# Performance work log

Measured on AMD Instinct MI355X. Metric: run time of the kernel, lower is better.

The kernel has to match this reference:

```python
import math
import jax, jax.numpy as jnp
import numpy as np

_EPS = 1e-6
N_DELTA, N_THETA, N_GAMMA = 4, 8, 16
N_OSC = N_DELTA + N_THETA + N_GAMMA  # 28
N_STEPS = 5
DT = 0.01
MATCH_THRESHOLD = 0.3
TWO_PI = 2.0 * math.pi

# Band natural frequencies (Hz): delta ~2, theta ~6, gamma ~40 (surrogate for DiscreteDeltaThetaGamma)
_OMEGA = TWO_PI * jnp.concatenate([
    jnp.full((N_DELTA,), 2.0, jnp.float32),
    jnp.full((N_THETA,), 6.0, jnp.float32),
    jnp.full((N_GAMMA,), 40.0, jnp.float32),
])


def setup_inputs() -> dict:
    key = jax.random.key(0)
    ks = jax.random.split(key, 12)
    N, D, H = 4096, 128, 64
    s1 = 1.0 / math.sqrt(D)
    s2 = 1.0 / math.sqrt(H)
    return {
        "detections_t": jax.random.normal(ks[0], (N, D), jnp.float32),
        "detections_t1": jax.random.normal(ks[1], (N, D), jnp.float32),
        # phase MLP
        "Wp1": jax.random.normal(ks[2], (D, H), jnp.float32) * s1,
        "bp1": jnp.zeros((H,), jnp.float32),
        "Wp2": jax.random.normal(ks[3], (H, N_OSC), jnp.float32) * s2,
        "bp2": jnp.zeros((N_OSC,), jnp.float32),
        # amplitude MLP
        "Wa1": jax.random.normal(ks[4], (D, H), jnp.float32) * s1,
        "ba1": jnp.zeros((H,), jnp.float32),
        "Wa2": jax.random.normal(ks[5], (H, N_OSC), jnp.float32) * s2,
        "ba2": jnp.zeros((N_OSC,), jnp.float32),
    }


def _encode(x, W1, b1, W2, b2, Wa1, ba1, Wa2, ba2):
    h = jax.nn.relu(x @ W1 + b1)
    phase = jnp.mod(h @ W2 + b2, TWO_PI)          # (N, n_osc)
    ha = jax.nn.relu(x @ Wa1 + ba1)
    amp = jax.nn.softplus(ha @ Wa2 + ba2)          # (N, n_osc)
    return phase, amp


def _evolve(phase, amp):
    # Kuramoto-style mean-field dynamics (surrogate for DiscreteDeltaThetaGamma.integrate)
    def step(carry, _):
        ph, am = carry
        c, s = jnp.cos(ph), jnp.sin(ph)
        mc = jnp.mean(c, axis=-1, keepdims=True)
        ms = jnp.mean(s, axis=-1, keepdims=True)
        # R*sin(psi - phi) = ms*cos(phi) - mc*sin(phi)
        coupling = ms * c - mc * s
        ph = jnp.mod(ph + DT * (_OMEGA + am * coupling), TWO_PI)
        return (ph, am), None
    (phase, amp), _ = jax.lax.scan(step, (phase, amp), None, length=N_STEPS)
    return phase, amp


def _phase_similarity(pa, pb):
    # sum_k cos(pa_k - pb_k) / (sqrt(K)+eps)^2, via real matmuls (no [Na,Nb,K] tensor)
    ca, sa = jnp.cos(pa), jnp.sin(pa)
    cb, sb = jnp.cos(pb), jnp.sin(pb)
    denom = (math.sqrt(N_OSC) + _EPS) ** 2
    return (ca @ cb.T + sa @ sb.T) / denom


def _greedy_match(sim, threshold):
    N_t, N_t1 = sim.shape
    max_sims = jnp.max(sim, axis=1)
    max_idxs = jnp.argmax(sim, axis=1)
    order = jnp.argsort(-max_sims)  # descending

    def step(used, idx):
        j = max_idxs[idx]
        ok = (~used[j]) & (max_sims[idx] > threshold)
        used = used.at[j].set(used[j] | ok)
        return used, jnp.where(ok, j, -1)

    used0 = jnp.zeros((N_t1,), bool)
    _, match_vals = jax.lax.scan(step, used0, order)
    matches = jnp.full((N_t,), -1, jnp.int32).at[order].set(match_vals.astype(jnp.int32))
    return matches


def reference(detections_t, detections_t1, Wp1, bp1, Wp2, bp2, Wa1, ba1, Wa2, ba2):
    phase_t, amp_t = _encode(detections_t, Wp1, bp1, Wp2, bp2, Wa1, ba1, Wa2, ba2)
    phase_t1, _ = _encode(detections_t1, Wp1, bp1, Wp2, bp2, Wa1, ba1, Wa2, ba2)
    phase_t_ev, _ = _evolve(phase_t, amp_t)
    sim = _phase_similarity(phase_t_ev, phase_t1)
    matches = _greedy_match(sim, MATCH_THRESHOLD)
    return matches, sim
```

## Files before the change

kernel.cpp:

```cpp
#include <hip/hip_runtime.h>
#include <math.h>

#define NDET 4096
#define DIM  128
#define HID  64
#define NOSC 28
#define KDIM 56

constexpr float TWO_PI_F = 6.28318530717958647692f;

__device__ __forceinline__ unsigned f2sort(float f){
    unsigned u = __float_as_uint(f);
    return (u & 0x80000000u) ? ~u : (u | 0x80000000u);
}
__device__ __forceinline__ float sort2f(unsigned u){
    return __uint_as_float((u & 0x80000000u) ? (u & 0x7fffffffu) : ~u);
}
__device__ __forceinline__ float lane_bcast(float v, int t){
    return __uint_as_float(__builtin_amdgcn_readlane(__float_as_uint(v), t));
}

__global__ __launch_bounds__(256) void encode_kernel(
    const float* __restrict__ det_t, const float* __restrict__ det_t1,
    const float* __restrict__ Wp1, const float* __restrict__ bp1,
    const float* __restrict__ Wp2, const float* __restrict__ bp2,
    const float* __restrict__ Wa1, const float* __restrict__ ba1,
    const float* __restrict__ Wa2, const float* __restrict__ ba2,
    float* __restrict__ At, float* __restrict__ Bt)
{
    const int tid  = threadIdx.x;
    const int lane = tid & 63;
    const int wv   = tid >> 6;
    const int b    = blockIdx.x;
    const bool isT = b < 512;
    const int lr = __builtin_amdgcn_readfirstlane(((b & 511) << 3) + wv * 2);
    const float* __restrict__ src = (isT ? det_t : det_t1) + (size_t)lr * DIM;

    float h0 = bp1[lane], h1 = h0;
    float g0 = 0.0f, g1 = 0.0f;
    if (isT){
        g0 = ba1[lane]; g1 = g0;
        #pragma unroll 8
        for (int d = 0; d < DIM; ++d){
            float x0 = src[d], x1 = src[DIM + d];
            float wp = Wp1[d * HID + lane];
            float wa = Wa1[d * HID + lane];
            h0 = fmaf(x0, wp, h0);  h1 = fmaf(x1, wp, h1);
            g0 = fmaf(x0, wa, g0);  g1 = fmaf(x1, wa, g1);
        }
        g0 = fmaxf(g0, 0.0f); g1 = fmaxf(g1, 0.0f);
    } else {
        #pragma unroll 8
        for (int d = 0; d < DIM; ++d){
            float x0 = src[d], x1 = src[DIM + d];
            float wp = Wp1[d * HID + lane];
            h0 = fmaf(x0, wp, h0);  h1 = fmaf(x1, wp, h1);
        }
    }
    h0 = fmaxf(h0, 0.0f); h1 = fmaxf(h1, 0.0f);

    const int k  = lane & 31;
    const bool kv = k < NOSC;
    const int kc = kv ? k : 0;

    float pa = bp2[kc], pb = pa;
    #pragma unroll 16
    for (int t = 0; t < HID; ++t){
        float w2 = Wp2[t * NOSC + kc];
        pa = fmaf(lane_bcast(h0, t), w2, pa);
        pb = fmaf(lane_bcast(h1, t), w2, pb);
    }
    float aa = 0.0f, ab = 0.0f;
    if (isT){
        aa = ba2[kc]; ab = aa;
        #pragma unroll 16
        for (int t = 0; t < HID; ++t){
            float w2 = Wa2[t * NOSC + kc];
            aa = fmaf(lane_bcast(g0, t), w2, aa);
            ab = fmaf(lane_bcast(g1, t), w2, ab);
        }
    }

    const bool hiHalf = lane >= 32;
    float p2 = hiHalf ? pb : pa;
    float ph = fmodf(p2, TWO_PI_F);
    if (ph < 0.0f) ph += TWO_PI_F;

    if (isT){
        float a2 = hiHalf ? ab : aa;
        float am = fmaxf(a2, 0.0f) + log1pf(expf(-fabsf(a2)));
        const float omega = TWO_PI_F * ((k < 4) ? 2.0f : (k < 12) ? 6.0f : 40.0f);
        for (int s5 = 0; s5 < 5; ++s5){
            float sn, cs;
            sincosf(ph, &sn, &cs);
            float c = kv ? cs : 0.0f;
            float s = kv ? sn : 0.0f;
            float sc = c, ss = s;
            sc += __shfl_xor(sc, 16); ss += __shfl_xor(ss, 16);
            sc += __shfl_xor(sc,  8); ss += __shfl_xor(ss,  8);
            sc += __shfl_xor(sc,  4); ss += __shfl_xor(ss,  4);
            sc += __shfl_xor(sc,  2); ss += __shfl_xor(ss,  2);
            sc += __shfl_xor(sc,  1); ss += __shfl_xor(ss,  1);
            float mc = sc * (1.0f / NOSC);
            float ms = ss * (1.0f / NOSC);
            float coupling = ms * c - mc * s;
            ph += 0.01f * (omega + am * coupling);
            ph = fmodf(ph, TWO_PI_F);
            if (ph < 0.0f) ph += TWO_PI_F;
        }
    }

    if (kv){
        const int row = lr + (hiHalf ? 1 : 0);
        float sn, cs;
        sincosf(ph, &sn, &cs);
        float* __restrict__ dst = isT ? At : Bt;
        dst[k * NDET + row]          = cs;
        dst[(NOSC + k) * NDET + row] = sn;
    }
}

__global__ __launch_bounds__(256, 4) void sim_kernel(
    const float* __restrict__ At, const float* __restrict__ Bt,
    float* __restrict__ sim_out, unsigned long long* __restrict__ rowmax)
{
    __shared__ float As[28][128];
    __shared__ float Bs[28][128];

    const int tid  = threadIdx.x;
    const int lane = tid & 63;
    const int wid  = tid >> 6;
    const int i0 = blockIdx.y * 128;
    const int j0 = blockIdx.x * 128;
    const int row0 = (wid & 1) * 64 + (lane & 7) * 8;
    const int col0 = (wid >> 1) * 64 + ((lane >> 3) & 7) * 8;

    float acc[8][8] = {};

    for (int chunk = 0; chunk < 2; ++chunk){
        const int kb = chunk * 28;
        if (chunk) __syncthreads();
        for (int v = tid; v < 28 * 32; v += 256){
            int kk = v >> 5, c4 = (v & 31) << 2;
            *(float4*)&As[kk][c4] = *(const float4*)&At[(size_t)(kb + kk) * NDET + i0 + c4];
            *(float4*)&Bs[kk][c4] = *(const float4*)&Bt[(size_t)(kb + kk) * NDET + j0 + c4];
        }
        __syncthreads();

        #pragma unroll 4
        for (int kk = 0; kk < 28; ++kk){
            float4 a0 = *(float4*)&As[kk][row0];
            float4 a1 = *(float4*)&As[kk][row0 + 4];
            float4 b0 = *(float4*)&Bs[kk][col0];
            float4 b1 = *(float4*)&Bs[kk][col0 + 4];
            float a[8]  = {a0.x, a0.y, a0.z, a0.w, a1.x, a1.y, a1.z, a1.w};
            float bb[8] = {b0.x, b0.y, b0.z, b0.w, b1.x, b1.y, b1.z, b1.w};
            #pragma unroll
            for (int r = 0; r < 8; ++r)
                #pragma unroll
                for (int c = 0; c < 8; ++c)
                    acc[r][c] = fmaf(a[r], bb[c], acc[r][c]);
        }
    }

    const float inv_denom =
        (float)(1.0 / ((5.2915026221291814 + 1e-6) * (5.2915026221291814 + 1e-6)));

    #pragma unroll
    for (int r = 0; r < 8; ++r){
        const int i = i0 + row0 + r;
        float vals[8];
        #pragma unroll
        for (int c = 0; c < 8; ++c) vals[c] = acc[r][c] * inv_denom;

        *(float4*)&sim_out[(size_t)i * NDET + j0 + col0]     =
            make_float4(vals[0], vals[1], vals[2], vals[3]);
        *(float4*)&sim_out[(size_t)i * NDET + j0 + col0 + 4] =
            make_float4(vals[4], vals[5], vals[6], vals[7]);

        float bv = vals[0]; int bj = j0 + col0;
        #pragma unroll
        for (int c = 1; c < 8; ++c)
            if (vals[c] > bv){ bv = vals[c]; bj = j0 + col0 + c; }
        unsigned long long key =
            ((unsigned long long)f2sort(bv) << 32) | (unsigned)(NDET - 1 - bj);
        #pragma unroll
        for (int m = 8; m <= 32; m <<= 1){
            unsigned long long o = __shfl_xor(key, m);
            if (o > key) key = o;
        }
        if (((lane >> 3) & 7) == 0) atomicMax(&rowmax[i], key);
    }
}

__global__ __launch_bounds__(256) void claim_kernel(
    const unsigned long long* __restrict__ rowmax,
    unsigned long long* __restrict__ colwin)
{
    int i = blockIdx.x * 256 + threadIdx.x;
    if (i >= NDET) return;
    unsigned long long key = rowmax[i];
    unsigned hi = (unsigned)(key >> 32);
    float v = sort2f(hi);
    if (v > 0.3f){
        int j = NDET - 1 - (int)(key & 0xffffffffu);
        unsigned long long ck = ((unsigned long long)hi << 32) | (unsigned)(NDET - 1 - i);
        atomicMax(&colwin[j], ck);
    }
}

__global__ __launch_bounds__(256) void finalize_kernel(
    const unsigned long long* __restrict__ rowmax,
    const unsigned long long* __restrict__ colwin,
    float* __restrict__ matches)
{
    int i = blockIdx.x * 256 + threadIdx.x;
    if (i >= NDET) return;
    unsigned long long key = rowmax[i];
    unsigned hi = (unsigned)(key >> 32);
    float v = sort2f(hi);
    int j = NDET - 1 - (int)(key & 0xffffffffu);
    unsigned long long ck = ((unsigned long long)hi << 32) | (unsigned)(NDET - 1 - i);
    bool ok = (v > 0.3f) && (colwin[j] == ck);
    matches[i] = ok ? (float)j : -1.0f;
}

extern "C" void kernel_launch(void* const* d_in, const int* in_sizes, int n_in,
                              void* d_out, int out_size, void* d_ws, size_t ws_size,
                              hipStream_t stream)
{
    const float* det_t  = (const float*)d_in[0];
    const float* det_t1 = (const float*)d_in[1];
    const float* Wp1 = (const float*)d_in[2];
    const float* bp1 = (const float*)d_in[3];
    const float* Wp2 = (const float*)d_in[4];
    const float* bp2 = (const float*)d_in[5];
    const float* Wa1 = (const float*)d_in[6];
    const float* ba1 = (const float*)d_in[7];
    const float* Wa2 = (const float*)d_in[8];
    const float* ba2 = (const float*)d_in[9];

    float* out     = (float*)d_out;
    float* matches = out;
    float* sim     = out + NDET;

    char* ws = (char*)d_ws;
    unsigned long long* rowmax = (unsigned long long*)ws;
    unsigned long long* colwin = (unsigned long long*)(ws + 32768);
    float* At = (float*)(ws + 65536);
    float* Bt = At + KDIM * NDET;

    hipMemsetAsync(d_ws, 0, 65536, stream);

    encode_kernel<<<1024, 256, 0, stream>>>(
        det_t, det_t1, Wp1, bp1, Wp2, bp2, Wa1, ba1, Wa2, ba2, At, Bt);

    sim_kernel<<<dim3(NDET / 128, NDET / 128), 256, 0, stream>>>(At, Bt, sim, rowmax);

    claim_kernel<<<NDET / 256, 256, 0, stream>>>(rowmax, colwin);
    finalize_kernel<<<NDET / 256, 256, 0, stream>>>(rowmax, colwin, matches);
}
```

Measured before the change: 157.8 us.

## Use split-fp16 MFMA for similarity GEMM and merge match kernels

The fp32 FMA similarity GEMM is replaced by MFMA 16x16x32 f16 instructions. Each operand is split into hi and lo fp16 parts and three products are summed to keep near-fp32 accuracy. The encode kernel now writes row-major fp16 hi/lo arrays padded to K=64, and sim_kernel loads fragments straight from global memory without LDS. The claim and finalize kernels are merged into one single-block kernel that keeps column winners in LDS, which removes a launch and part of the memset. The risk is that the split-fp16 precision error could flip the argmax on near-ties.

```diff
diff --git a/kernel.cpp b/kernel.cpp
--- a/kernel.cpp
+++ b/kernel.cpp
@@ -5,9 +5,12 @@
 #define DIM  128
 #define HID  64
 #define NOSC 28
-#define KDIM 56
+#define KPAD 64
 
 constexpr float TWO_PI_F = 6.28318530717958647692f;
+
+typedef _Float16 f16x8 __attribute__((ext_vector_type(8)));
+typedef float    f32x4 __attribute__((ext_vector_type(4)));
 
 __device__ __forceinline__ unsigned f2sort(float f){
     unsigned u = __float_as_uint(f);
@@ -26,7 +29,8 @@
     const float* __restrict__ Wp2, const float* __restrict__ bp2,
     const float* __restrict__ Wa1, const float* __restrict__ ba1,
     const float* __restrict__ Wa2, const float* __restrict__ ba2,
-    float* __restrict__ At, float* __restrict__ Bt)
+    _Float16* __restrict__ Ahi, _Float16* __restrict__ Alo,
+    _Float16* __restrict__ Bhi, _Float16* __restrict__ Blo)
 {
     const int tid  = threadIdx.x;
     const int lane = tid & 63;
@@ -110,119 +114,146 @@
         }
     }
 
+    const int row = lr + (hiHalf ? 1 : 0);
+    _Float16* __restrict__ dhi = isT ? Ahi : Bhi;
+    _Float16* __restrict__ dlo = isT ? Alo : Blo;
+    const size_t rb = (size_t)row * KPAD;
     if (kv){
-        const int row = lr + (hiHalf ? 1 : 0);
         float sn, cs;
         sincosf(ph, &sn, &cs);
-        float* __restrict__ dst = isT ? At : Bt;
-        dst[k * NDET + row]          = cs;
-        dst[(NOSC + k) * NDET + row] = sn;
-    }
-}
-
-__global__ __launch_bounds__(256, 4) void sim_kernel(
-    const float* __restrict__ At, const float* __restrict__ Bt,
+        _Float16 ch = (_Float16)cs;
+        _Float16 sh = (_Float16)sn;
+        _Float16 cl = (_Float16)(cs - (float)ch);
+        _Float16 sl = (_Float16)(sn - (float)sh);
+        dhi[rb + k]        = ch;
+        dhi[rb + NOSC + k] = sh;
+        dlo[rb + k]        = cl;
+        dlo[rb + NOSC + k] = sl;
+    } else {
+        const int kk = k - NOSC;
+        dhi[rb + 56 + kk] = (_Float16)0.0f;
+        dhi[rb + 60 + kk] = (_Float16)0.0f;
+        dlo[rb + 56 + kk] = (_Float16)0.0f;
+        dlo[rb + 60 + kk] = (_Float16)0.0f;
+    }
+}
+
+__global__ __launch_bounds__(256) void sim_kernel(
+    const _Float16* __restrict__ Ahi, const _Float16* __restrict__ Alo,
+    const _Float16* __restrict__ Bhi, const _Float16* __restrict__ Blo,
     float* __restrict__ sim_out, unsigned long long* __restrict__ rowmax)
 {
-    __shared__ float As[28][128];
-    __shared__ float Bs[28][128];
-
     const int tid  = threadIdx.x;
     const int lane = tid & 63;
     const int wid  = tid >> 6;
-    const int i0 = blockIdx.y * 128;
-    const int j0 = blockIdx.x * 128;
-    const int row0 = (wid & 1) * 64 + (lane & 7) * 8;
-    const int col0 = (wid >> 1) * 64 + ((lane >> 3) & 7) * 8;
-
-    float acc[8][8] = {};
-
-    for (int chunk = 0; chunk < 2; ++chunk){
-        const int kb = chunk * 28;
-        if (chunk) __syncthreads();
-        for (int v = tid; v < 28 * 32; v += 256){
-            int kk = v >> 5, c4 = (v & 31) << 2;
-            *(float4*)&As[kk][c4] = *(const float4*)&At[(size_t)(kb + kk) * NDET + i0 + c4];
-            *(float4*)&Bs[kk][c4] = *(const float4*)&Bt[(size_t)(kb + kk) * NDET + j0 + c4];
-        }
-        __syncthreads();
-
-        #pragma unroll 4
-        for (int kk = 0; kk < 28; ++kk){
-            float4 a0 = *(float4*)&As[kk][row0];
-            float4 a1 = *(float4*)&As[kk][row0 + 4];
-            float4 b0 = *(float4*)&Bs[kk][col0];
-            float4 b1 = *(float4*)&Bs[kk][col0 + 4];
-            float a[8]  = {a0.x, a0.y, a0.z, a0.w, a1.x, a1.y, a1.z, a1.w};
-            float bb[8] = {b0.x, b0.y, b0.z, b0.w, b1.x, b1.y, b1.z, b1.w};
-            #pragma unroll
-            for (int r = 0; r < 8; ++r)
-                #pragma unroll
-                for (int c = 0; c < 8; ++c)
-                    acc[r][c] = fmaf(a[r], bb[c], acc[r][c]);
-        }
-    }
+    const int i0 = blockIdx.y * 128 + (wid & 1) * 64;
+    const int j0 = blockIdx.x * 128 + (wid >> 1) * 64;
+    const int r16 = lane & 15;
+    const int g   = lane >> 4;
+
+    f16x8 ahi[4][2], alo[4][2];
+    #pragma unroll
+    for (int ib = 0; ib < 4; ++ib)
+        #pragma unroll
+        for (int kc = 0; kc < 2; ++kc){
+            const size_t off = (size_t)(i0 + ib*16 + r16) * KPAD + kc*32 + g*8;
+            ahi[ib][kc] = *(const f16x8*)&Ahi[off];
+            alo[ib][kc] = *(const f16x8*)&Alo[off];
+        }
 
     const float inv_denom =
         (float)(1.0 / ((5.2915026221291814 + 1e-6) * (5.2915026221291814 + 1e-6)));
 
-    #pragma unroll
-    for (int r = 0; r < 8; ++r){
-        const int i = i0 + row0 + r;
-        float vals[8];
-        #pragma unroll
-        for (int c = 0; c < 8; ++c) vals[c] = acc[r][c] * inv_denom;
-
-        *(float4*)&sim_out[(size_t)i * NDET + j0 + col0]     =
-            make_float4(vals[0], vals[1], vals[2], vals[3]);
-        *(float4*)&sim_out[(size_t)i * NDET + j0 + col0 + 4] =
-            make_float4(vals[4], vals[5], vals[6], vals[7]);
-
-        float bv = vals[0]; int bj = j0 + col0;
-        #pragma unroll
-        for (int c = 1; c < 8; ++c)
-            if (vals[c] > bv){ bv = vals[c]; bj = j0 + col0 + c; }
+    float bv[4] = {-3.4e38f, -3.4e38f, -3.4e38f, -3.4e38f};
+    int   bj[4] = {0, 0, 0, 0};
+
+    #pragma unroll 1
+    for (int jb = 0; jb < 4; ++jb){
+        f16x8 bhi[2], blo[2];
+        #pragma unroll
+        for (int kc = 0; kc < 2; ++kc){
+            const size_t off = (size_t)(j0 + jb*16 + r16) * KPAD + kc*32 + g*8;
+            bhi[kc] = *(const f16x8*)&Bhi[off];
+            blo[kc] = *(const f16x8*)&Blo[off];
+        }
+
+        f32x4 acc[4] = {};
+        #pragma unroll
+        for (int ib = 0; ib < 4; ++ib){
+            #pragma unroll
+            for (int kc = 0; kc < 2; ++kc){
+                acc[ib] = __builtin_amdgcn_mfma_f32_16x16x32_f16(bhi[kc], alo[ib][kc], acc[ib], 0, 0, 0);
+                acc[ib] = __builtin_amdgcn_mfma_f32_16x16x32_f16(blo[kc], ahi[ib][kc], acc[ib], 0, 0, 0);
+                acc[ib] = __builtin_amdgcn_mfma_f32_16x16x32_f16(bhi[kc], ahi[ib][kc], acc[ib], 0, 0, 0);
+            }
+        }
+
+        #pragma unroll
+        for (int ib = 0; ib < 4; ++ib){
+            const int i = i0 + ib*16 + r16;
+            f32x4 v = acc[ib];
+            float4 out = make_float4(v[0]*inv_denom, v[1]*inv_denom,
+                                     v[2]*inv_denom, v[3]*inv_denom);
+            *(float4*)&sim_out[(size_t)i * NDET + j0 + jb*16 + g*4] = out;
+            float vv[4] = {out.x, out.y, out.z, out.w};
+            #pragma unroll
+            for (int r = 0; r < 4; ++r){
+                if (vv[r] > bv[ib]){ bv[ib] = vv[r]; bj[ib] = j0 + jb*16 + g*4 + r; }
+            }
+        }
+    }
+
+    #pragma unroll
+    for (int ib = 0; ib < 4; ++ib){
+        const int i = i0 + ib*16 + r16;
         unsigned long long key =
-            ((unsigned long long)f2sort(bv) << 32) | (unsigned)(NDET - 1 - bj);
-        #pragma unroll
-        for (int m = 8; m <= 32; m <<= 1){
-            unsigned long long o = __shfl_xor(key, m);
-            if (o > key) key = o;
-        }
-        if (((lane >> 3) & 7) == 0) atomicMax(&rowmax[i], key);
-    }
-}
-
-__global__ __launch_bounds__(256) void claim_kernel(
+            ((unsigned long long)f2sort(bv[ib]) << 32) | (unsigned)(NDET - 1 - bj[ib]);
+        unsigned long long o;
+        o = __shfl_xor(key, 16); if (o > key) key = o;
+        o = __shfl_xor(key, 32); if (o > key) key = o;
+        if (g == 0) atomicMax(&rowmax[i], key);
+    }
+}
+
+__global__ __launch_bounds__(1024) void match_kernel(
     const unsigned long long* __restrict__ rowmax,
-    unsigned long long* __restrict__ colwin)
-{
-    int i = blockIdx.x * 256 + threadIdx.x;
-    if (i >= NDET) return;
-    unsigned long long key = rowmax[i];
-    unsigned hi = (unsigned)(key >> 32);
-    float v = sort2f(hi);
-    if (v > 0.3f){
+    float* __restrict__ matches)
+{
+    __shared__ unsigned long long colwin[NDET];
+    const int tid = threadIdx.x;
+
+    #pragma unroll
+    for (int t = 0; t < 4; ++t) colwin[tid + t*1024] = 0ull;
+    __syncthreads();
+
+    unsigned long long keys[4];
+    #pragma unroll
+    for (int t = 0; t < 4; ++t){
+        const int i = tid + t*1024;
+        unsigned long long key = rowmax[i];
+        keys[t] = key;
+        unsigned hi = (unsigned)(key >> 32);
+        float v = sort2f(hi);
+        if (v > 0.3f){
+            int j = NDET - 1 - (int)(key & 0xffffffffu);
+            unsigned long long ck =
+                ((unsigned long long)hi << 32) | (unsigned)(NDET - 1 - i);
+            atomicMax(&colwin[j], ck);
+        }
+    }
+    __syncthreads();
+
+    #pragma unroll
+    for (int t = 0; t < 4; ++t){
+        const int i = tid + t*1024;
+        unsigned long long key = keys[t];
+        unsigned hi = (unsigned)(key >> 32);
+        float v = sort2f(hi);
         int j = NDET - 1 - (int)(key & 0xffffffffu);
-        unsigned long long ck = ((unsigned long long)hi << 32) | (unsigned)(NDET - 1 - i);
-        atomicMax(&colwin[j], ck);
-    }
-}
-
-__global__ __launch_bounds__(256) void finalize_kernel(
-    const unsigned long long* __restrict__ rowmax,
-    const unsigned long long* __restrict__ colwin,
-    float* __restrict__ matches)
-{
-    int i = blockIdx.x * 256 + threadIdx.x;
-    if (i >= NDET) return;
-    unsigned long long key = rowmax[i];
-    unsigned hi = (unsigned)(key >> 32);
-    float v = sort2f(hi);
-    int j = NDET - 1 - (int)(key & 0xffffffffu);
-    unsigned long long ck = ((unsigned long long)hi << 32) | (unsigned)(NDET - 1 - i);
-    bool ok = (v > 0.3f) && (colwin[j] == ck);
-    matches[i] = ok ? (float)j : -1.0f;
+        unsigned long long ck =
+            ((unsigned long long)hi << 32) | (unsigned)(NDET - 1 - i);
+        matches[i] = (v > 0.3f && colwin[j] == ck) ? (float)j : -1.0f;
+    }
 }
 
 extern "C" void kernel_launch(void* const* d_in, const int* in_sizes, int n_in,
@@ -246,17 +277,18 @@
 
     char* ws = (char*)d_ws;
     unsigned long long* rowmax = (unsigned long long*)ws;
-    unsigned long long* colwin = (unsigned long long*)(ws + 32768);
-    float* At = (float*)(ws + 65536);
-    float* Bt = At + KDIM * NDET;
-
-    hipMemsetAsync(d_ws, 0, 65536, stream);
+    _Float16* Ahi = (_Float16*)(ws + 32768);
+    _Float16* Alo = Ahi + (size_t)NDET * KPAD;
+    _Float16* Bhi = Alo + (size_t)NDET * KPAD;
+    _Float16* Blo = Bhi + (size_t)NDET * KPAD;
+
+    hipMemsetAsync(d_ws, 0, 32768, stream);
 
     encode_kernel<<<1024, 256, 0, stream>>>(
-        det_t, det_t1, Wp1, bp1, Wp2, bp2, Wa1, ba1, Wa2, ba2, At, Bt);
-
-    sim_kernel<<<dim3(NDET / 128, NDET / 128), 256, 0, stream>>>(At, Bt, sim, rowmax);
-
-    claim_kernel<<<NDET / 256, 256, 0, stream>>>(rowmax, colwin);
-    finalize_kernel<<<NDET / 256, 256, 0, stream>>>(rowmax, colwin, matches);
-}
+        det_t, det_t1, Wp1, bp1, Wp2, bp2, Wa1, ba1, Wa2, ba2, Ahi, Alo, Bhi, Blo);
+
+    sim_kernel<<<dim3(NDET / 128, NDET / 128), 256, 0, stream>>>(
+        Ahi, Alo, Bhi, Blo, sim, rowmax);
+
+    match_kernel<<<1, 1024, 0, stream>>>(rowmax, matches);
+}
```

New measurement: 128.1 us. 1.23x faster.
